# Kernel tuning notes

Hardware: AMD Instinct MI355X
Metric: run time of the kernel (lower is better)

The kernel has to match this reference:

```python
import jax, jax.numpy as jnp
import numpy as np

NUM_LOCS = 32000
LOC_EMB = 512
TIM_EMB = 64
HID = 1024
SEQ = 2048
INP = LOC_EMB + TIM_EMB  # 576
NEG = -1.0e11


def setup_inputs() -> dict:
    key = jax.random.key(0)
    ks = jax.random.split(key, 10)
    sc = 0.02
    return {
        "loc": jax.random.randint(ks[0], (1, SEQ), 0, NUM_LOCS),
        "tim": jax.random.randint(ks[1], (1, SEQ), 0, 48),
        "emb_loc": jax.random.normal(ks[2], (NUM_LOCS + 1, LOC_EMB), jnp.float32) * sc,
        "emb_tim": jax.random.normal(ks[3], (48, TIM_EMB), jnp.float32) * sc,
        "W_ih": jax.random.normal(ks[4], (4 * HID, INP), jnp.float32) * sc,
        "W_hh": jax.random.normal(ks[5], (4 * HID, HID), jnp.float32) * sc,
        "b_ih": jnp.zeros((4 * HID,), jnp.float32),
        "b_hh": jnp.zeros((4 * HID,), jnp.float32),
        "W_fc": jax.random.normal(ks[6], (NUM_LOCS + 1, 2 * HID), jnp.float32) * sc,
        "b_fc": jnp.zeros((NUM_LOCS + 1,), jnp.float32),
    }


def _lstm(x, W_ih, W_hh, b_ih, b_hh):
    # x: [S, INP]  (batch==1, squeezed). PyTorch gate order: i, f, g, o.
    H = W_hh.shape[1]
    xg = x @ W_ih.T + (b_ih + b_hh)  # [S, 4H] precompute input projections

    def step(carry, xt):
        h, c = carry
        z = xt + h @ W_hh.T
        i, f, g, o = jnp.split(z, 4)
        c = jax.nn.sigmoid(f) * c + jax.nn.sigmoid(i) * jnp.tanh(g)
        h = jax.nn.sigmoid(o) * jnp.tanh(c)
        return (h, c), h

    h0 = jnp.zeros((H,), x.dtype)
    _, hs = jax.lax.scan(step, (h0, h0), xg)
    return hs  # [S, H]


def reference(loc, tim, emb_loc, emb_tim, W_ih, W_hh, b_ih, b_hh, W_fc, b_fc):
    # embeddings -> [1, S, INP] -> [S, INP] (batch 1, dropout is identity in eval)
    x = jnp.concatenate([emb_loc[loc], emb_tim[tim]], axis=-1)[0]
    hs = _lstm(x, W_ih, W_hh, b_ih, b_hh)  # [S, H]
    # dot attention: energies[i,j] = hs[i] . hs[j], causal mask (tril keep, strict-upper = -1e11)
    energies = hs @ hs.T  # [S, S]
    S = energies.shape[0]
    causal = jnp.tril(jnp.ones((S, S), bool))
    energies = jnp.where(causal, energies, jnp.asarray(NEG, energies.dtype))
    attn = jax.nn.softmax(energies, axis=-1)
    context = attn @ hs  # [S, H]
    out = jnp.concatenate([hs, context], axis=-1)  # [S, 2H]
    y = out @ W_fc.T + b_fc  # [S, NUM_LOCS+1]
    return jax.nn.log_softmax(y, axis=-1)
```

## Files before the change

kernel.cpp:

```cpp
#include <hip/hip_runtime.h>
#include <hip/hip_bf16.h>

#define SEQ   2048
#define HID   1024
#define INP   576
#define G4H   4096
#define NOUT  32001

typedef __attribute__((ext_vector_type(8))) short bf16x8;
typedef __attribute__((ext_vector_type(4))) float f32x4;

__device__ __forceinline__ unsigned short f2bf(float f) {
  unsigned int u = __builtin_bit_cast(unsigned int, f);
  unsigned int r = (u + 0x7FFFu + ((u >> 16) & 1u)) >> 16;
  return (unsigned short)r;
}
__device__ __forceinline__ float bf2f(unsigned short h) {
  unsigned int u = ((unsigned int)h) << 16;
  return __builtin_bit_cast(float, u);
}

__global__ __launch_bounds__(128)
void k_embed(const int* __restrict__ loc, const int* __restrict__ tim,
             const float* __restrict__ el, const float* __restrict__ et,
             unsigned short* __restrict__ xbf) {
  int s = blockIdx.x;
  int l = loc[s], t = tim[s];
  for (int c = threadIdx.x; c < INP; c += 128) {
    float v = (c < 512) ? el[(size_t)l * 512 + c] : et[(size_t)t * 64 + (c - 512)];
    xbf[(size_t)s * INP + c] = f2bf(v);
  }
}

template<int BSRC, int OUTBF, int TRI>
__global__ __launch_bounds__(256)
void k_gemm(const unsigned short* __restrict__ A, int lda,
            const void* __restrict__ B, int ldb,
            void* __restrict__ C, long long ldc, long long cofs,
            int M, int N, int K,
            const float* __restrict__ bias0, const float* __restrict__ bias1) {
  int m0 = blockIdx.x * 128;
  int n0 = blockIdx.y * 128;
  if (TRI && n0 > m0 + 127) return;

  __shared__ unsigned short sA[128][40];
  __shared__ unsigned short sB[128][40];

  int tid = threadIdx.x;
  int lane = tid & 63;
  int wid = tid >> 6;
  int wm = (wid >> 1) * 64, wn = (wid & 1) * 64;
  int r16 = lane & 15, quad = lane >> 4;

  f32x4 acc[4][4];
#pragma unroll
  for (int i = 0; i < 4; ++i)
#pragma unroll
    for (int j = 0; j < 4; ++j)
#pragma unroll
      for (int r = 0; r < 4; ++r) acc[i][j][r] = 0.f;

  int nk = K / 32;
  for (int kt = 0; kt < nk; ++kt) {
    int k0 = kt * 32;
#pragma unroll
    for (int h = 0; h < 2; ++h) {
      int c = tid + h * 256;
      int row = c >> 2, part = c & 3;
      bf16x8 av = *(const bf16x8*)(A + (size_t)(m0 + row) * lda + k0 + part * 8);
      *(bf16x8*)&sA[row][part * 8] = av;
    }
#pragma unroll
    for (int h = 0; h < 2; ++h) {
      int c = tid + h * 256;
      int row = c >> 2, part = c & 3;
      int gr = n0 + row;
      bf16x8 bv;
      if (gr < N) {
        if (BSRC == 0) {
          bv = *(const bf16x8*)((const unsigned short*)B + (size_t)gr * ldb + k0 + part * 8);
        } else {
          const float* bp = (const float*)B + (size_t)gr * ldb + k0 + part * 8;
          f32x4 b0 = *(const f32x4*)bp;
          f32x4 b1 = *(const f32x4*)(bp + 4);
#pragma unroll
          for (int z = 0; z < 4; ++z) bv[z] = (short)f2bf(b0[z]);
#pragma unroll
          for (int z = 0; z < 4; ++z) bv[4 + z] = (short)f2bf(b1[z]);
        }
      } else {
#pragma unroll
        for (int z = 0; z < 8; ++z) bv[z] = 0;
      }
      *(bf16x8*)&sB[row][part * 8] = bv;
    }
    __syncthreads();
    bf16x8 af[4], bfr[4];
#pragma unroll
    for (int i = 0; i < 4; ++i) {
      af[i]  = *(const bf16x8*)&sA[wm + i * 16 + r16][quad * 8];
      bfr[i] = *(const bf16x8*)&sB[wn + i * 16 + r16][quad * 8];
    }
#pragma unroll
    for (int i = 0; i < 4; ++i)
#pragma unroll
      for (int j = 0; j < 4; ++j)
        acc[i][j] = __builtin_amdgcn_mfma_f32_16x16x32_bf16(af[i], bfr[j], acc[i][j], 0, 0, 0);
    __syncthreads();
  }

#pragma unroll
  for (int i = 0; i < 4; ++i) {
    int rowb = m0 + wm + i * 16 + quad * 4;
#pragma unroll
    for (int j = 0; j < 4; ++j) {
      int col = n0 + wn + j * 16 + r16;
      if (col >= N) continue;
      float b = 0.f;
      if (bias0) b += bias0[col];
      if (bias1) b += bias1[col];
#pragma unroll
      for (int r = 0; r < 4; ++r) {
        float v = acc[i][j][r] + b;
        size_t idx = (size_t)(rowb + r) * (size_t)ldc + (size_t)cofs + col;
        if (OUTBF) ((unsigned short*)C)[idx] = f2bf(v);
        else       ((float*)C)[idx] = v;
      }
    }
  }
}

__global__ __launch_bounds__(256)
void k_lstm(const float* __restrict__ Whh, const float* __restrict__ xg,
            unsigned int* __restrict__ hglob,
            unsigned short* __restrict__ hs_bf, unsigned short* __restrict__ hsT_bf,
            unsigned short* __restrict__ out_bf) {
  __shared__ unsigned short sW[16][1024];
  __shared__ float sH[1024];
  __shared__ float sZ[16];

  int blk = blockIdx.x;
  int tid = threadIdx.x;
  int r = tid >> 4, kl = tid & 15;

  {
    int q = r >> 2, j = r & 3;
    int gr = q * HID + blk * 4 + j;
    const float* wrow = Whh + (size_t)gr * HID;
    for (int c = kl * 64; c < kl * 64 + 64; c += 4) {
      f32x4 w = *(const f32x4*)(wrow + c);
      sW[r][c]     = f2bf(w[0]);
      sW[r][c + 1] = f2bf(w[1]);
      sW[r][c + 2] = f2bf(w[2]);
      sW[r][c + 3] = f2bf(w[3]);
    }
  }
  float cst = 0.f;
  __syncthreads();

  int gr_row = (r >> 2) * HID + blk * 4 + (r & 3);

  for (int t = 0; t < SEQ; ++t) {
    float xgv = 0.f;
    if (kl == 0) xgv = xg[(size_t)t * G4H + gr_row];

    if (t == 0) {
      for (int i = tid; i < HID; i += 256) sH[i] = 0.f;
    } else {
      const unsigned int* src = hglob + (size_t)(t - 1) * HID;
      unsigned int want = (unsigned int)t;
#pragma unroll
      for (int i = 0; i < 4; ++i) {
        int idx = tid * 4 + i;
        unsigned int v;
        do {
          v = __hip_atomic_load(&src[idx], __ATOMIC_RELAXED, __HIP_MEMORY_SCOPE_AGENT);
        } while ((v >> 16) != want);
        sH[idx] = bf2f((unsigned short)(v & 0xFFFFu));
      }
    }
    __syncthreads();

    float acc = 0.f;
#pragma unroll
    for (int kk = 0; kk < 8; ++kk) {
      int k0 = (kk * 16 + kl) * 8;
      bf16x8 wv = *(const bf16x8*)&sW[r][k0];
#pragma unroll
      for (int z = 0; z < 8; ++z)
        acc += bf2f((unsigned short)wv[z]) * sH[k0 + z];
    }
    acc += __shfl_xor(acc, 1);
    acc += __shfl_xor(acc, 2);
    acc += __shfl_xor(acc, 4);
    acc += __shfl_xor(acc, 8);
    if (kl == 0) sZ[r] = acc + xgv;
    __syncthreads();

    if (tid < 4) {
      int j = tid;
      float zi = sZ[j], zf = sZ[4 + j], zg = sZ[8 + j], zo = sZ[12 + j];
      float gi = 1.f / (1.f + __expf(-zi));
      float gf = 1.f / (1.f + __expf(-zf));
      float gg = tanhf(zg);
      float go = 1.f / (1.f + __expf(-zo));
      cst = gf * cst + gi * gg;
      float h = go * tanhf(cst);
      unsigned short hb = f2bf(h);
      int gj = blk * 4 + j;
      __hip_atomic_store(&hglob[(size_t)t * HID + gj],
                         (((unsigned int)(t + 1)) << 16) | (unsigned int)hb,
                         __ATOMIC_RELAXED, __HIP_MEMORY_SCOPE_AGENT);
      hs_bf[(size_t)t * HID + gj] = hb;
      hsT_bf[(size_t)gj * SEQ + t] = hb;
      out_bf[(size_t)t * (2 * HID) + gj] = hb;
    }
  }
}

__global__ __launch_bounds__(256)
void k_softmax(const float* __restrict__ E, unsigned short* __restrict__ P) {
  int i = blockIdx.x;
  int n = i + 1;
  const float* e = E + (size_t)i * SEQ;
  __shared__ float red[4];
  int tid = threadIdx.x, lane = tid & 63, w = tid >> 6;

  float m = -1e30f;
  for (int j = tid; j < n; j += 256) m = fmaxf(m, e[j]);
  for (int o = 32; o; o >>= 1) m = fmaxf(m, __shfl_xor(m, o));
  if (lane == 0) red[w] = m;
  __syncthreads();
  m = fmaxf(fmaxf(red[0], red[1]), fmaxf(red[2], red[3]));
  __syncthreads();

  float s = 0.f;
  for (int j = tid; j < n; j += 256) s += __expf(e[j] - m);
  for (int o = 32; o; o >>= 1) s += __shfl_xor(s, o);
  if (lane == 0) red[w] = s;
  __syncthreads();
  s = red[0] + red[1] + red[2] + red[3];
  float inv = 1.f / s;

  unsigned short* p = P + (size_t)i * SEQ;
  for (int j = tid; j < SEQ; j += 256)
    p[j] = (j < n) ? f2bf(__expf(e[j] - m) * inv) : (unsigned short)0;
}

__global__ __launch_bounds__(256)
void k_logsoftmax(float* __restrict__ Y) {
  int i = blockIdx.x;
  float* y = Y + (size_t)i * (size_t)NOUT;
  __shared__ float red[4];
  int tid = threadIdx.x, lane = tid & 63, w = tid >> 6;

  float m = -1e30f;
  for (int j = tid; j < NOUT; j += 256) m = fmaxf(m, y[j]);
  for (int o = 32; o; o >>= 1) m = fmaxf(m, __shfl_xor(m, o));
  if (lane == 0) red[w] = m;
  __syncthreads();
  m = fmaxf(fmaxf(red[0], red[1]), fmaxf(red[2], red[3]));
  __syncthreads();

  float s = 0.f;
  for (int j = tid; j < NOUT; j += 256) s += __expf(y[j] - m);
  for (int o = 32; o; o >>= 1) s += __shfl_xor(s, o);
  if (lane == 0) red[w] = s;
  __syncthreads();
  s = red[0] + red[1] + red[2] + red[3];
  float lse = m + logf(s);

  for (int j = tid; j < NOUT; j += 256) y[j] -= lse;
}

extern "C" void kernel_launch(void* const* d_in, const int* in_sizes, int n_in,
                              void* d_out, int out_size, void* d_ws, size_t ws_size,
                              hipStream_t stream) {
  (void)in_sizes; (void)n_in; (void)out_size; (void)ws_size;
  const int*   loc     = (const int*)d_in[0];
  const int*   tim     = (const int*)d_in[1];
  const float* emb_loc = (const float*)d_in[2];
  const float* emb_tim = (const float*)d_in[3];
  const float* W_ih    = (const float*)d_in[4];
  const float* W_hh    = (const float*)d_in[5];
  const float* b_ih    = (const float*)d_in[6];
  const float* b_hh    = (const float*)d_in[7];
  const float* W_fc    = (const float*)d_in[8];
  const float* b_fc    = (const float*)d_in[9];

  char* ws = (char*)d_ws;
  size_t off = 0;
  auto alloc = [&](size_t bytes) {
    void* p = ws + off;
    off += (bytes + 255) & ~(size_t)255;
    return p;
  };
  unsigned short* xbf    = (unsigned short*)alloc((size_t)SEQ * INP * 2);
  float*          xg     = (float*)         alloc((size_t)SEQ * G4H * 4);
  unsigned int*   hglob  = (unsigned int*)  alloc((size_t)SEQ * HID * 4);
  unsigned short* hs_bf  = (unsigned short*)alloc((size_t)SEQ * HID * 2);
  unsigned short* hsT_bf = (unsigned short*)alloc((size_t)HID * SEQ * 2);
  float*          energ  = (float*)         alloc((size_t)SEQ * SEQ * 4);
  unsigned short* attn   = (unsigned short*)alloc((size_t)SEQ * SEQ * 2);
  unsigned short* out_bf = (unsigned short*)alloc((size_t)SEQ * 2 * HID * 2);
  float*          y      = (float*)d_out;

  k_embed<<<SEQ, 128, 0, stream>>>(loc, tim, emb_loc, emb_tim, xbf);

  k_gemm<1, 0, 0><<<dim3(SEQ / 128, G4H / 128), 256, 0, stream>>>(
      xbf, INP, W_ih, INP, xg, G4H, 0, SEQ, G4H, INP, b_ih, b_hh);

  k_lstm<<<256, 256, 0, stream>>>(W_hh, xg, hglob, hs_bf, hsT_bf, out_bf);

  k_gemm<0, 0, 1><<<dim3(SEQ / 128, SEQ / 128), 256, 0, stream>>>(
      hs_bf, HID, hs_bf, HID, energ, SEQ, 0, SEQ, SEQ, HID, nullptr, nullptr);

  k_softmax<<<SEQ, 256, 0, stream>>>(energ, attn);

  k_gemm<0, 1, 0><<<dim3(SEQ / 128, HID / 128), 256, 0, stream>>>(
      attn, SEQ, hsT_bf, SEQ, out_bf, 2 * HID, HID, SEQ, HID, SEQ, nullptr, nullptr);

  k_gemm<1, 0, 0><<<dim3(SEQ / 128, (NOUT + 127) / 128), 256, 0, stream>>>(
      out_bf, 2 * HID, W_fc, 2 * HID, y, NOUT, 0, SEQ, NOUT, 2 * HID, b_fc, nullptr);

  k_logsoftmax<<<SEQ, 256, 0, stream>>>(y);
}
```

Baseline: 7.139 ms.

## Keep LSTM recurrent weights in registers, fast gate math, online logsoftmax

The persistent LSTM kernel now keeps each thread's 64 fp32 W_hh weights in registers instead of bf16 LDS rows. The per-step dot product is split across waves, then reduced with two shuffles and a small shared partial array. The h-vector polling loop now loads four words per check, and the gate nonlinearities use rcp/exp approximations computed in parallel across 16 lanes. Separately, logsoftmax switches to a single-pass online max/sum, removing one full read of the large output matrix, at the cost of extra exps.

```diff
diff --git a/kernel.cpp b/kernel.cpp
--- a/kernel.cpp
+++ b/kernel.cpp
@@ -18,6 +18,12 @@
 __device__ __forceinline__ float bf2f(unsigned short h) {
   unsigned int u = ((unsigned int)h) << 16;
   return __builtin_bit_cast(float, u);
+}
+__device__ __forceinline__ float sigm_fast(float x) {
+  return __builtin_amdgcn_rcpf(1.f + __expf(-x));
+}
+__device__ __forceinline__ float tanh_fast(float x) {
+  return 1.f - 2.f * __builtin_amdgcn_rcpf(1.f + __expf(2.f * x));
 }
 
 __global__ __launch_bounds__(128)
@@ -135,85 +141,88 @@
             unsigned int* __restrict__ hglob,
             unsigned short* __restrict__ hs_bf, unsigned short* __restrict__ hsT_bf,
             unsigned short* __restrict__ out_bf) {
-  __shared__ unsigned short sW[16][1024];
   __shared__ float sH[1024];
-  __shared__ float sZ[16];
+  __shared__ float sP[4][16];
 
   int blk = blockIdx.x;
   int tid = threadIdx.x;
-  int r = tid >> 4, kl = tid & 15;
-
+  int r = tid & 15, kl = tid >> 4;
+  int gr_row = (r >> 2) * HID + blk * 4 + (r & 3);
+
+  float wreg[64];
   {
-    int q = r >> 2, j = r & 3;
-    int gr = q * HID + blk * 4 + j;
-    const float* wrow = Whh + (size_t)gr * HID;
-    for (int c = kl * 64; c < kl * 64 + 64; c += 4) {
-      f32x4 w = *(const f32x4*)(wrow + c);
-      sW[r][c]     = f2bf(w[0]);
-      sW[r][c + 1] = f2bf(w[1]);
-      sW[r][c + 2] = f2bf(w[2]);
-      sW[r][c + 3] = f2bf(w[3]);
+    const float* wrow = Whh + (size_t)gr_row * HID + kl * 64;
+#pragma unroll
+    for (int c = 0; c < 16; ++c) {
+      f32x4 w = *(const f32x4*)(wrow + c * 4);
+      wreg[c * 4 + 0] = w[0]; wreg[c * 4 + 1] = w[1];
+      wreg[c * 4 + 2] = w[2]; wreg[c * 4 + 3] = w[3];
     }
   }
   float cst = 0.f;
-  __syncthreads();
-
-  int gr_row = (r >> 2) * HID + blk * 4 + (r & 3);
 
   for (int t = 0; t < SEQ; ++t) {
     float xgv = 0.f;
-    if (kl == 0) xgv = xg[(size_t)t * G4H + gr_row];
+    if (tid < 16) xgv = xg[(size_t)t * G4H + (tid >> 2) * HID + blk * 4 + (tid & 3)];
 
     if (t == 0) {
-      for (int i = tid; i < HID; i += 256) sH[i] = 0.f;
+      f32x4 z4 = {0.f, 0.f, 0.f, 0.f};
+      *(f32x4*)&sH[tid * 4] = z4;
     } else {
-      const unsigned int* src = hglob + (size_t)(t - 1) * HID;
+      const unsigned int* src = hglob + (size_t)(t - 1) * HID + tid * 4;
       unsigned int want = (unsigned int)t;
-#pragma unroll
-      for (int i = 0; i < 4; ++i) {
-        int idx = tid * 4 + i;
-        unsigned int v;
-        do {
-          v = __hip_atomic_load(&src[idx], __ATOMIC_RELAXED, __HIP_MEMORY_SCOPE_AGENT);
-        } while ((v >> 16) != want);
-        sH[idx] = bf2f((unsigned short)(v & 0xFFFFu));
+      unsigned int v0, v1, v2, v3;
+      for (;;) {
+        v0 = __hip_atomic_load(src + 0, __ATOMIC_RELAXED, __HIP_MEMORY_SCOPE_AGENT);
+        v1 = __hip_atomic_load(src + 1, __ATOMIC_RELAXED, __HIP_MEMORY_SCOPE_AGENT);
+        v2 = __hip_atomic_load(src + 2, __ATOMIC_RELAXED, __HIP_MEMORY_SCOPE_AGENT);
+        v3 = __hip_atomic_load(src + 3, __ATOMIC_RELAXED, __HIP_MEMORY_SCOPE_AGENT);
+        if (((v0 >> 16) == want) & ((v1 >> 16) == want) &
+            ((v2 >> 16) == want) & ((v3 >> 16) == want)) break;
       }
+      f32x4 hv;
+      hv[0] = bf2f((unsigned short)(v0 & 0xFFFFu));
+      hv[1] = bf2f((unsigned short)(v1 & 0xFFFFu));
+      hv[2] = bf2f((unsigned short)(v2 & 0xFFFFu));
+      hv[3] = bf2f((unsigned short)(v3 & 0xFFFFu));
+      *(f32x4*)&sH[tid * 4] = hv;
     }
     __syncthreads();
 
     float acc = 0.f;
 #pragma unroll
-    for (int kk = 0; kk < 8; ++kk) {
-      int k0 = (kk * 16 + kl) * 8;
-      bf16x8 wv = *(const bf16x8*)&sW[r][k0];
-#pragma unroll
-      for (int z = 0; z < 8; ++z)
-        acc += bf2f((unsigned short)wv[z]) * sH[k0 + z];
-    }
-    acc += __shfl_xor(acc, 1);
-    acc += __shfl_xor(acc, 2);
-    acc += __shfl_xor(acc, 4);
-    acc += __shfl_xor(acc, 8);
-    if (kl == 0) sZ[r] = acc + xgv;
+    for (int c = 0; c < 16; ++c) {
+      f32x4 hv = *(const f32x4*)&sH[kl * 64 + c * 4];
+      acc += wreg[c * 4 + 0] * hv[0] + wreg[c * 4 + 1] * hv[1] +
+             wreg[c * 4 + 2] * hv[2] + wreg[c * 4 + 3] * hv[3];
+    }
+    acc += __shfl_xor(acc, 16, 64);
+    acc += __shfl_xor(acc, 32, 64);
+    int lane = tid & 63, w = tid >> 6;
+    if (lane < 16) sP[w][lane] = acc;
     __syncthreads();
 
-    if (tid < 4) {
-      int j = tid;
-      float zi = sZ[j], zf = sZ[4 + j], zg = sZ[8 + j], zo = sZ[12 + j];
-      float gi = 1.f / (1.f + __expf(-zi));
-      float gf = 1.f / (1.f + __expf(-zf));
-      float gg = tanhf(zg);
-      float go = 1.f / (1.f + __expf(-zo));
-      cst = gf * cst + gi * gg;
-      float h = go * tanhf(cst);
-      unsigned short hb = f2bf(h);
-      int gj = blk * 4 + j;
-      __hip_atomic_store(&hglob[(size_t)t * HID + gj],
-                         (((unsigned int)(t + 1)) << 16) | (unsigned int)hb,
-                         __ATOMIC_RELAXED, __HIP_MEMORY_SCOPE_AGENT);
-      hs_bf[(size_t)t * HID + gj] = hb;
-      hsT_bf[(size_t)gj * SEQ + t] = hb;
-      out_bf[(size_t)t * (2 * HID) + gj] = hb;
+    if (tid < 16) {
+      float z = sP[0][tid] + sP[1][tid] + sP[2][tid] + sP[3][tid] + xgv;
+      int q = tid >> 2;
+      float a = (q == 2) ? tanh_fast(z) : sigm_fast(z);
+      int j = tid & 3;
+      float gi = __shfl(a, j, 64);
+      float gf = __shfl(a, 4 + j, 64);
+      float gg = __shfl(a, 8 + j, 64);
+      float go = __shfl(a, 12 + j, 64);
+      if (tid < 4) {
+        cst = gf * cst + gi * gg;
+        float h = go * tanh_fast(cst);
+        unsigned short hb = f2bf(h);
+        int gj = blk * 4 + j;
+        __hip_atomic_store(&hglob[(size_t)t * HID + gj],
+                           (((unsigned int)(t + 1)) << 16) | (unsigned int)hb,
+                           __ATOMIC_RELAXED, __HIP_MEMORY_SCOPE_AGENT);
+        hs_bf[(size_t)t * HID + gj] = hb;
+        hsT_bf[(size_t)gj * SEQ + t] = hb;
+        out_bf[(size_t)t * (2 * HID) + gj] = hb;
+      }
     }
   }
 }
@@ -251,25 +260,35 @@
 void k_logsoftmax(float* __restrict__ Y) {
   int i = blockIdx.x;
   float* y = Y + (size_t)i * (size_t)NOUT;
-  __shared__ float red[4];
+  __shared__ float redm[4], reds[4];
   int tid = threadIdx.x, lane = tid & 63, w = tid >> 6;
 
-  float m = -1e30f;
-  for (int j = tid; j < NOUT; j += 256) m = fmaxf(m, y[j]);
-  for (int o = 32; o; o >>= 1) m = fmaxf(m, __shfl_xor(m, o));
-  if (lane == 0) red[w] = m;
-  __syncthreads();
-  m = fmaxf(fmaxf(red[0], red[1]), fmaxf(red[2], red[3]));
-  __syncthreads();
-
-  float s = 0.f;
-  for (int j = tid; j < NOUT; j += 256) s += __expf(y[j] - m);
-  for (int o = 32; o; o >>= 1) s += __shfl_xor(s, o);
-  if (lane == 0) red[w] = s;
-  __syncthreads();
-  s = red[0] + red[1] + red[2] + red[3];
-  float lse = m + logf(s);
-
+  float m = -1e30f, s = 0.f;
+  for (int j = tid; j < NOUT; j += 256) {
+    float v = y[j];
+    float nm = fmaxf(m, v);
+    s = s * __expf(m - nm) + __expf(v - nm);
+    m = nm;
+  }
+  for (int o = 32; o; o >>= 1) {
+    float om = __shfl_xor(m, o), os = __shfl_xor(s, o);
+    float nm = fmaxf(m, om);
+    s = s * __expf(m - nm) + os * __expf(om - nm);
+    m = nm;
+  }
+  if (lane == 0) { redm[w] = m; reds[w] = s; }
+  __syncthreads();
+  if (tid == 0) {
+    float fm = redm[0], fs = reds[0];
+    for (int k = 1; k < 4; ++k) {
+      float nm = fmaxf(fm, redm[k]);
+      fs = fs * __expf(fm - nm) + reds[k] * __expf(redm[k] - nm);
+      fm = nm;
+    }
+    redm[0] = fm + logf(fs);
+  }
+  __syncthreads();
+  float lse = redm[0];
   for (int j = tid; j < NOUT; j += 256) y[j] -= lse;
 }
 
```

Measured after the change: 6.274 ms. 12.1% less time.
